# Performance work log

Measured on AMD Instinct MI355X. Metric: run time of the kernel, lower is better.

The kernel has to match this reference:

```python
import jax, jax.numpy as jnp
import numpy as np

B, C, H, W = 1, 256, 96, 96   # inplanes=256
P = 64                        # planes=64


def setup_inputs() -> dict:
    key = jax.random.key(0)
    ks = jax.random.split(key, 8)
    x = jax.random.normal(ks[0], (B, C, H, W), dtype=jnp.float32)
    y = jax.random.normal(ks[1], (B, C, H, W), dtype=jnp.float32)
    # 1x1 convs == channel matmuls; torch init: normal(0, 0.01), zero bias
    Wv = 0.01 * jax.random.normal(ks[2], (C, C), dtype=jnp.float32)  # conv_value (no bias)
    Wq = 0.01 * jax.random.normal(ks[3], (P, C), dtype=jnp.float32)
    bq = jnp.zeros((P,), dtype=jnp.float32)
    Wk = 0.01 * jax.random.normal(ks[4], (P, C), dtype=jnp.float32)
    bk = jnp.zeros((P,), dtype=jnp.float32)
    # gamma initializes to 0 in the module; use 0.5 so the output is nontrivial
    gamma = jnp.full((1,), 0.5, dtype=jnp.float32)
    return {"x": x, "y": y, "Wv": Wv, "Wq": Wq, "bq": bq, "Wk": Wk, "bk": bk, "gamma": gamma}


def reference(x, y, Wv, Wq, bq, Wk, bk, gamma):
    b, c, h, w = x.shape
    n = h * w                       # query positions (from x)
    m = y.shape[2] * y.shape[3]     # key/value positions (from y)
    xf = x.reshape(b, c, n)         # [B, C, N]
    yf = y.reshape(b, c, m)         # [B, C, M]

    value = jnp.einsum('oc,bcm->bom', Wv, yf)                    # [B, C, M]
    query = jnp.einsum('pc,bcn->bpn', Wq, xf) + bq[None, :, None]  # [B, P, N]
    key_ = jnp.einsum('pc,bcm->bpm', Wk, yf) + bk[None, :, None]   # [B, P, M]

    # mean-centering over spatial dim
    query = query - query.mean(axis=2, keepdims=True)
    key_ = key_ - key_.mean(axis=2, keepdims=True)

    sim = jnp.einsum('bpn,bpm->bnm', query, key_)   # [B, N, M]
    sim = jax.nn.softmax(sim, axis=2)
    out = jnp.einsum('bnm,bcm->bcn', sim, value)    # [B, C, N]
    out = out.reshape(b, c, h, w)
    return gamma[0] * out
```

## Files before the change

### kernel.cpp

```cpp
#include <hip/hip_runtime.h>


typedef __attribute__((ext_vector_type(8))) short short8;
typedef __attribute__((ext_vector_type(8))) unsigned short ushort8;
typedef __attribute__((ext_vector_type(4))) float f32x4;

#define C_DIM 256
#define P_DIM 64
#define N_DIM 9216
#define NT    144
#define SPLITS 4
#define MQ    (N_DIM / SPLITS)
#define KV_TILES (MQ / 64)

__device__ __forceinline__ unsigned short f2b(float f) {
  unsigned int u = __float_as_uint(f);
  u += 0x7fffu + ((u >> 16) & 1u);
  return (unsigned short)(u >> 16);
}

__device__ __forceinline__ float b2f(unsigned short h) {
  return __uint_as_float(((unsigned int)h) << 16);
}

__device__ __forceinline__ f32x4 mfma16(short8 a, short8 b, f32x4 c) {
  return __builtin_amdgcn_mfma_f32_16x16x32_bf16(a, b, c, 0, 0, 0);
}

__global__ void k1_mean_conv(const float* __restrict__ x, const float* __restrict__ y,
                             unsigned short* __restrict__ xb, unsigned short* __restrict__ yb,
                             float* __restrict__ xmean, float* __restrict__ ymean) {
  int b = blockIdx.x;
  const float* src = (b < C_DIM) ? x : y;
  unsigned short* dst = (b < C_DIM) ? xb : yb;
  float* mout = (b < C_DIM) ? xmean : ymean;
  int c = b & (C_DIM - 1);
  const float4* row = (const float4*)(src + (size_t)c * N_DIM);
  ushort4* orow = (ushort4*)(dst + (size_t)c * N_DIM);
  int tid = threadIdx.x;
  float s = 0.f;
  for (int i = tid; i < N_DIM / 4; i += 256) {
    float4 v = row[i];
    s += v.x + v.y + v.z + v.w;
    ushort4 o;
    o.x = f2b(v.x); o.y = f2b(v.y); o.z = f2b(v.z); o.w = f2b(v.w);
    orow[i] = o;
  }
#pragma unroll
  for (int off = 1; off < 64; off <<= 1) s += __shfl_xor(s, off);
  __shared__ float red[4];
  if ((tid & 63) == 0) red[tid >> 6] = s;
  __syncthreads();
  if (tid == 0) mout[c] = (red[0] + red[1] + red[2] + red[3]) * (1.f / (float)N_DIM);
}

__global__ void k2_wconv(const float* __restrict__ Wv, const float* __restrict__ Wq,
                         const float* __restrict__ Wk,
                         const float* __restrict__ xmean, const float* __restrict__ ymean,
                         unsigned short* __restrict__ Wvb, unsigned short* __restrict__ Wqb,
                         unsigned short* __restrict__ Wkb,
                         float* __restrict__ qmean, float* __restrict__ kmean) {
  int b = blockIdx.x, t = threadIdx.x;
  if (b < 256) {
    int i = b * 256 + t; Wvb[i] = f2b(Wv[i]);
  } else if (b < 320) {
    int i = (b - 256) * 256 + t; Wqb[i] = f2b(Wq[i]);
  } else if (b < 384) {
    int i = (b - 320) * 256 + t; Wkb[i] = f2b(Wk[i]);
  } else if (t < 128) {
    int p = t & 63;
    const float* W = (t < 64) ? Wq : Wk;
    const float* mv = (t < 64) ? xmean : ymean;
    float s = 0.f;
    for (int cc = 0; cc < 256; cc++) s += W[p * 256 + cc] * mv[cc];
    ((t < 64) ? qmean : kmean)[p] = s;
  }
}

__global__ void k3_proj(const unsigned short* __restrict__ xb, const unsigned short* __restrict__ yb,
                        const unsigned short* __restrict__ Wvb, const unsigned short* __restrict__ Wqb,
                        const unsigned short* __restrict__ Wkb,
                        const float* __restrict__ qmean, const float* __restrict__ kmean,
                        unsigned short* __restrict__ Qb, unsigned short* __restrict__ Kb,
                        unsigned short* __restrict__ Vb) {
  __shared__ unsigned short T[64][264];
  int b = blockIdx.x;
  int role = b / NT;
  int tile = b % NT;
  int m0 = tile * 64;
  int tid = threadIdx.x;
  int w = tid >> 6, lane = tid & 63, l16 = lane & 15, g4 = lane >> 4;

  const unsigned short* src = (role == 1) ? xb : yb;
  {
    int c = tid;
    const unsigned short* sr = src + (size_t)c * N_DIM + m0;
#pragma unroll
    for (int j = 0; j < 8; j++) {
      ushort8 v = *(const ushort8*)&sr[j * 8];
#pragma unroll
      for (int i = 0; i < 8; i++) T[j * 8 + i][c] = v[i];
    }
  }
  __syncthreads();

  if (role == 0) {
    f32x4 acc[4][4];
#pragma unroll
    for (int rf = 0; rf < 4; rf++)
#pragma unroll
      for (int cf = 0; cf < 4; cf++) acc[rf][cf] = (f32x4)0.f;
#pragma unroll
    for (int kk = 0; kk < 8; kk++) {
      short8 bf[4];
#pragma unroll
      for (int cf = 0; cf < 4; cf++)
        bf[cf] = *(const short8*)&T[cf * 16 + l16][kk * 32 + g4 * 8];
#pragma unroll
      for (int rf = 0; rf < 4; rf++) {
        short8 af = *(const short8*)&Wvb[(size_t)(w * 64 + rf * 16 + l16) * 256 + kk * 32 + g4 * 8];
#pragma unroll
        for (int cf = 0; cf < 4; cf++) acc[rf][cf] = mfma16(af, bf[cf], acc[rf][cf]);
      }
    }
#pragma unroll
    for (int rf = 0; rf < 4; rf++)
#pragma unroll
      for (int cf = 0; cf < 4; cf++)
#pragma unroll
        for (int r = 0; r < 4; r++) {
          int co = w * 64 + rf * 16 + g4 * 4 + r;
          int m = m0 + cf * 16 + l16;
          Vb[(size_t)co * N_DIM + m] = f2b(acc[rf][cf][r]);
        }
  } else {
    const unsigned short* Wb = (role == 1) ? Wqb : Wkb;
    const float* mean = (role == 1) ? qmean : kmean;
    unsigned short* Ob = (role == 1) ? Qb : Kb;
    f32x4 acc[4];
#pragma unroll
    for (int cf = 0; cf < 4; cf++) acc[cf] = (f32x4)0.f;
#pragma unroll
    for (int kk = 0; kk < 8; kk++) {
      short8 af = *(const short8*)&T[w * 16 + l16][kk * 32 + g4 * 8];
#pragma unroll
      for (int cf = 0; cf < 4; cf++) {
        short8 bf = *(const short8*)&Wb[(size_t)(cf * 16 + l16) * 256 + kk * 32 + g4 * 8];
        acc[cf] = mfma16(af, bf, acc[cf]);
      }
    }
#pragma unroll
    for (int cf = 0; cf < 4; cf++)
#pragma unroll
      for (int r = 0; r < 4; r++) {
        int n = m0 + w * 16 + g4 * 4 + r;
        int p = cf * 16 + l16;
        Ob[(size_t)n * 64 + p] = f2b(acc[cf][r] - mean[p]);
      }
  }
}

__global__ __launch_bounds__(256, 2)
void k4_attn(const unsigned short* __restrict__ Qb, const unsigned short* __restrict__ Kb,
             const unsigned short* __restrict__ Vb,
             unsigned short* __restrict__ po, float* __restrict__ m_arr, float* __restrict__ l_arr) {
  __shared__ unsigned short Kt[64][72];
  __shared__ unsigned short Vt[256][72];
  __shared__ unsigned short Pt[64][72];

  int b = blockIdx.x;
  int s = b & (SPLITS - 1);
  int n0 = (b >> 2) * 64;
  int tid = threadIdx.x;
  int w = tid >> 6, lane = tid & 63, l16 = lane & 15, g4 = lane >> 4;

  short8 qf[2];
  {
    const unsigned short* qrow = Qb + (size_t)(n0 + w * 16 + l16) * 64;
    qf[0] = *(const short8*)&qrow[g4 * 8];
    qf[1] = *(const short8*)&qrow[32 + g4 * 8];
  }

  f32x4 acc[16];
#pragma unroll
  for (int i = 0; i < 16; i++) acc[i] = (f32x4)0.f;
  float mreg[4], lreg[4];
#pragma unroll
  for (int r = 0; r < 4; r++) { mreg[r] = -3e38f; lreg[r] = 0.f; }

  for (int t = 0; t < KV_TILES; t++) {
    int m0 = s * MQ + t * 64;
    for (int idx = tid; idx < 64 * 8; idx += 256) {
      int r = idx >> 3, j = idx & 7;
      *(ushort8*)&Kt[r][j * 8] = *(const ushort8*)&Kb[(size_t)(m0 + r) * 64 + j * 8];
    }
    for (int idx = tid; idx < 256 * 8; idx += 256) {
      int r = idx >> 3, j = idx & 7;
      *(ushort8*)&Vt[r][j * 8] = *(const ushort8*)&Vb[(size_t)r * N_DIM + m0 + j * 8];
    }
    __syncthreads();

    f32x4 sa[4];
#pragma unroll
    for (int cf = 0; cf < 4; cf++) sa[cf] = (f32x4)0.f;
#pragma unroll
    for (int kk = 0; kk < 2; kk++) {
#pragma unroll
      for (int cf = 0; cf < 4; cf++) {
        short8 kf = *(const short8*)&Kt[cf * 16 + l16][kk * 32 + g4 * 8];
        sa[cf] = mfma16(qf[kk], kf, sa[cf]);
      }
    }

    float f[4];
#pragma unroll
    for (int r = 0; r < 4; r++) {
      float v = fmaxf(fmaxf(sa[0][r], sa[1][r]), fmaxf(sa[2][r], sa[3][r]));
#pragma unroll
      for (int off = 1; off < 16; off <<= 1) v = fmaxf(v, __shfl_xor(v, off));
      float mnew = fmaxf(mreg[r], v);
      f[r] = __expf(mreg[r] - mnew);
      mreg[r] = mnew;
    }
    float p[4][4];
#pragma unroll
    for (int cf = 0; cf < 4; cf++)
#pragma unroll
      for (int r = 0; r < 4; r++) p[cf][r] = __expf(sa[cf][r] - mreg[r]);
#pragma unroll
    for (int r = 0; r < 4; r++) {
      float sv = p[0][r] + p[1][r] + p[2][r] + p[3][r];
#pragma unroll
      for (int off = 1; off < 16; off <<= 1) sv += __shfl_xor(sv, off);
      lreg[r] = lreg[r] * f[r] + sv;
    }
#pragma unroll
    for (int cfc = 0; cfc < 16; cfc++)
#pragma unroll
      for (int r = 0; r < 4; r++) acc[cfc][r] *= f[r];

#pragma unroll
    for (int cf = 0; cf < 4; cf++)
#pragma unroll
      for (int r = 0; r < 4; r++)
        Pt[w * 16 + g4 * 4 + r][cf * 16 + l16] = f2b(p[cf][r]);

#pragma unroll
    for (int kk = 0; kk < 2; kk++) {
      short8 pf = *(const short8*)&Pt[w * 16 + l16][kk * 32 + g4 * 8];
#pragma unroll
      for (int cfc = 0; cfc < 16; cfc++) {
        short8 vf = *(const short8*)&Vt[cfc * 16 + l16][kk * 32 + g4 * 8];
        acc[cfc] = mfma16(pf, vf, acc[cfc]);
      }
    }
    __syncthreads();
  }

  unsigned short* poS = po + (size_t)s * N_DIM * C_DIM;
#pragma unroll
  for (int cfc = 0; cfc < 16; cfc++)
#pragma unroll
    for (int r = 0; r < 4; r++) {
      int n = n0 + w * 16 + g4 * 4 + r;
      int c = cfc * 16 + l16;
      poS[(size_t)n * C_DIM + c] = f2b(acc[cfc][r]);
    }
  if (l16 == 0) {
#pragma unroll
    for (int r = 0; r < 4; r++) {
      int n = n0 + w * 16 + g4 * 4 + r;
      m_arr[s * N_DIM + n] = mreg[r];
      l_arr[s * N_DIM + n] = lreg[r];
    }
  }
}

__global__ void k5_combine(const unsigned short* __restrict__ po, const float* __restrict__ m_arr,
                           const float* __restrict__ l_arr, const float* __restrict__ gamma,
                           float* __restrict__ out) {
  __shared__ float TT[64][65];
  int b = blockIdx.x;
  int c0 = (b & 3) * 64;
  int n0 = (b >> 2) * 64;
  float g = gamma[0];
  int tid = threadIdx.x;
#pragma unroll
  for (int rr = 0; rr < 16; rr++) {
    int idx = rr * 256 + tid;
    int nl = idx >> 6, cl = idx & 63;
    int n = n0 + nl;
    float m0v = m_arr[n], m1v = m_arr[N_DIM + n];
    float m2v = m_arr[2 * N_DIM + n], m3v = m_arr[3 * N_DIM + n];
    float M = fmaxf(fmaxf(m0v, m1v), fmaxf(m2v, m3v));
    float w0 = __expf(m0v - M), w1 = __expf(m1v - M);
    float w2 = __expf(m2v - M), w3 = __expf(m3v - M);
    float denom = l_arr[n] * w0 + l_arr[N_DIM + n] * w1 +
                  l_arr[2 * N_DIM + n] * w2 + l_arr[3 * N_DIM + n] * w3;
    float v0 = b2f(po[(size_t)n * C_DIM + c0 + cl]);
    float v1 = b2f(po[((size_t)N_DIM + n) * C_DIM + c0 + cl]);
    float v2 = b2f(po[((size_t)2 * N_DIM + n) * C_DIM + c0 + cl]);
    float v3 = b2f(po[((size_t)3 * N_DIM + n) * C_DIM + c0 + cl]);
    TT[cl][nl] = (v0 * w0 + v1 * w1 + v2 * w2 + v3 * w3) / denom;
  }
  __syncthreads();
#pragma unroll
  for (int rr = 0; rr < 16; rr++) {
    int idx = rr * 256 + tid;
    int cl = idx >> 6, nl = idx & 63;
    out[(size_t)(c0 + cl) * N_DIM + n0 + nl] = g * TT[cl][nl];
  }
}

extern "C" void kernel_launch(void* const* d_in, const int* in_sizes, int n_in,
                              void* d_out, int out_size, void* d_ws, size_t ws_size,
                              hipStream_t stream) {
  const float* x  = (const float*)d_in[0];
  const float* y  = (const float*)d_in[1];
  const float* Wv = (const float*)d_in[2];
  const float* Wq = (const float*)d_in[3];
  const float* Wk = (const float*)d_in[5];
  const float* gamma = (const float*)d_in[7];
  float* out = (float*)d_out;

  char* ws = (char*)d_ws;
  constexpr size_t OFF_XMEAN = 0;
  constexpr size_t OFF_YMEAN = 1024;
  constexpr size_t OFF_QMEAN = 2048;
  constexpr size_t OFF_KMEAN = 2560;
  constexpr size_t OFF_XB    = 4096;
  constexpr size_t OFF_YB    = OFF_XB + 4718592;
  constexpr size_t OFF_WVB   = OFF_YB + 4718592;
  constexpr size_t OFF_WQB   = OFF_WVB + 131072;
  constexpr size_t OFF_WKB   = OFF_WQB + 32768;
  constexpr size_t OFF_QB    = OFF_WKB + 32768;
  constexpr size_t OFF_KB    = OFF_QB + 1179648;
  constexpr size_t OFF_VB    = OFF_KB + 1179648;
  constexpr size_t OFF_PO    = OFF_VB + 4718592;
  constexpr size_t OFF_M     = OFF_PO + (size_t)SPLITS * N_DIM * C_DIM * 2;
  constexpr size_t OFF_L     = OFF_M + (size_t)SPLITS * N_DIM * 4;

  float* xmean = (float*)(ws + OFF_XMEAN);
  float* ymean = (float*)(ws + OFF_YMEAN);
  float* qmean = (float*)(ws + OFF_QMEAN);
  float* kmean = (float*)(ws + OFF_KMEAN);
  unsigned short* xb  = (unsigned short*)(ws + OFF_XB);
  unsigned short* yb  = (unsigned short*)(ws + OFF_YB);
  unsigned short* Wvb = (unsigned short*)(ws + OFF_WVB);
  unsigned short* Wqb = (unsigned short*)(ws + OFF_WQB);
  unsigned short* Wkb = (unsigned short*)(ws + OFF_WKB);
  unsigned short* Qb  = (unsigned short*)(ws + OFF_QB);
  unsigned short* Kb  = (unsigned short*)(ws + OFF_KB);
  unsigned short* Vb  = (unsigned short*)(ws + OFF_VB);
  unsigned short* po  = (unsigned short*)(ws + OFF_PO);
  float* m_arr = (float*)(ws + OFF_M);
  float* l_arr = (float*)(ws + OFF_L);

  k1_mean_conv<<<512, 256, 0, stream>>>(x, y, xb, yb, xmean, ymean);
  k2_wconv<<<385, 256, 0, stream>>>(Wv, Wq, Wk, xmean, ymean, Wvb, Wqb, Wkb, qmean, kmean);
  k3_proj<<<432, 256, 0, stream>>>(xb, yb, Wvb, Wqb, Wkb, qmean, kmean, Qb, Kb, Vb);
  k4_attn<<<NT * SPLITS, 256, 0, stream>>>(Qb, Kb, Vb, po, m_arr, l_arr);
  k5_combine<<<576, 256, 0, stream>>>(po, m_arr, l_arr, gamma, out);
}
```

Measured before the change: 356.3 us.

## Prefetch V tiles into registers and read K fragments directly from global

The attention kernel now register-prefetches the next V tile, one row per thread, while computing the current tile's scores. This overlaps global load latency with the MFMA and softmax work. K fragments are read straight from global memory instead of being staged through shared memory, which frees LDS. Launch bounds rise to three blocks per SU, which increases register pressure (the kernel holds 64 accumulator floats plus 8 prefetch vectors) and risks spills. Direct K reads from global may be less coalesced.

Measured after the change: 405.4 us. 13.8% more time.

```diff
diff --git a/kernel.cpp b/kernel.cpp
--- a/kernel.cpp
+++ b/kernel.cpp
@@ -160,11 +160,10 @@
   }
 }
 
-__global__ __launch_bounds__(256, 2)
+__global__ __launch_bounds__(256, 3)
 void k4_attn(const unsigned short* __restrict__ Qb, const unsigned short* __restrict__ Kb,
              const unsigned short* __restrict__ Vb,
              unsigned short* __restrict__ po, float* __restrict__ m_arr, float* __restrict__ l_arr) {
-  __shared__ unsigned short Kt[64][72];
   __shared__ unsigned short Vt[256][72];
   __shared__ unsigned short Pt[64][72];
 
@@ -188,16 +187,20 @@
 #pragma unroll
   for (int r = 0; r < 4; r++) { mreg[r] = -3e38f; lreg[r] = 0.f; }
 
+  int mbase = s * MQ;
+
+  ushort8 vreg[8];
+  {
+    const ushort8* vsrc = (const ushort8*)(Vb + (size_t)tid * N_DIM + mbase);
+#pragma unroll
+    for (int j = 0; j < 8; j++) vreg[j] = vsrc[j];
+  }
+
   for (int t = 0; t < KV_TILES; t++) {
-    int m0 = s * MQ + t * 64;
-    for (int idx = tid; idx < 64 * 8; idx += 256) {
-      int r = idx >> 3, j = idx & 7;
-      *(ushort8*)&Kt[r][j * 8] = *(const ushort8*)&Kb[(size_t)(m0 + r) * 64 + j * 8];
-    }
-    for (int idx = tid; idx < 256 * 8; idx += 256) {
-      int r = idx >> 3, j = idx & 7;
-      *(ushort8*)&Vt[r][j * 8] = *(const ushort8*)&Vb[(size_t)r * N_DIM + m0 + j * 8];
-    }
+    int m0 = mbase + t * 64;
+    if (t) __syncthreads();
+#pragma unroll
+    for (int j = 0; j < 8; j++) *(ushort8*)&Vt[tid][j * 8] = vreg[j];
     __syncthreads();
 
     f32x4 sa[4];
@@ -207,9 +210,15 @@
     for (int kk = 0; kk < 2; kk++) {
 #pragma unroll
       for (int cf = 0; cf < 4; cf++) {
-        short8 kf = *(const short8*)&Kt[cf * 16 + l16][kk * 32 + g4 * 8];
+        short8 kf = *(const short8*)&Kb[(size_t)(m0 + cf * 16 + l16) * 64 + kk * 32 + g4 * 8];
         sa[cf] = mfma16(qf[kk], kf, sa[cf]);
       }
+    }
+
+    if (t + 1 < KV_TILES) {
+      const ushort8* vsrc = (const ushort8*)(Vb + (size_t)tid * N_DIM + m0 + 64);
+#pragma unroll
+      for (int j = 0; j < 8; j++) vreg[j] = vsrc[j];
     }
 
     float f[4];
@@ -222,14 +231,13 @@
       f[r] = __expf(mreg[r] - mnew);
       mreg[r] = mnew;
     }
-    float p[4][4];
 #pragma unroll
     for (int cf = 0; cf < 4; cf++)
 #pragma unroll
-      for (int r = 0; r < 4; r++) p[cf][r] = __expf(sa[cf][r] - mreg[r]);
+      for (int r = 0; r < 4; r++) sa[cf][r] = __expf(sa[cf][r] - mreg[r]);
 #pragma unroll
     for (int r = 0; r < 4; r++) {
-      float sv = p[0][r] + p[1][r] + p[2][r] + p[3][r];
+      float sv = sa[0][r] + sa[1][r] + sa[2][r] + sa[3][r];
 #pragma unroll
       for (int off = 1; off < 16; off <<= 1) sv += __shfl_xor(sv, off);
       lreg[r] = lreg[r] * f[r] + sv;
@@ -243,7 +251,7 @@
     for (int cf = 0; cf < 4; cf++)
 #pragma unroll
       for (int r = 0; r < 4; r++)
-        Pt[w * 16 + g4 * 4 + r][cf * 16 + l16] = f2b(p[cf][r]);
+        Pt[w * 16 + g4 * 4 + r][cf * 16 + l16] = f2b(sa[cf][r]);
 
 #pragma unroll
     for (int kk = 0; kk < 2; kk++) {
@@ -254,7 +262,6 @@
         acc[cfc] = mfma16(pf, vf, acc[cfc]);
       }
     }
-    __syncthreads();
   }
 
   unsigned short* poS = po + (size_t)s * N_DIM * C_DIM;
```
